# Kernel tuning notes

Hardware: AMD Instinct MI355X
Metric: run time of the kernel (lower is better)

## Reference

```python
import jax, jax.numpy as jnp
import numpy as np

B, S, D, H, DFF = 2, 4096, 768, 12, 3072
DH = D // H
EPS = 1e-6


def layer_norm(x, gamma, beta):
    # torch.std is unbiased (ddof=1); normalizer is (sigma + eps), NOT sqrt(var+eps)
    mu = jnp.mean(x, axis=-1, keepdims=True)
    sigma = jnp.sqrt(jnp.var(x, axis=-1, keepdims=True, ddof=1))
    return gamma * (x - mu) / (sigma + EPS) + beta


def setup_inputs() -> dict:
    key = jax.random.key(0)
    ks = jax.random.split(key, 12)
    sc = 1.0 / np.sqrt(D)
    inp = {
        "x": jax.random.normal(ks[0], (B, S, D), dtype=jnp.float32),
        "mask": jnp.ones((B, S, S), dtype=jnp.float32),  # multiplicative mask
        "wq": jax.random.normal(ks[1], (D, D), dtype=jnp.float32) * sc,
        "bq": jnp.zeros((D,), dtype=jnp.float32),
        "wk": jax.random.normal(ks[2], (D, D), dtype=jnp.float32) * sc,
        "bk": jnp.zeros((D,), dtype=jnp.float32),
        "wv": jax.random.normal(ks[3], (D, D), dtype=jnp.float32) * sc,
        "bv": jnp.zeros((D,), dtype=jnp.float32),
        "wo": jax.random.normal(ks[4], (D, D), dtype=jnp.float32) * sc,
        "bo": jnp.zeros((D,), dtype=jnp.float32),
        "w1": jax.random.normal(ks[5], (D, DFF), dtype=jnp.float32) * sc,
        "b1": jnp.zeros((DFF,), dtype=jnp.float32),
        "w2": jax.random.normal(ks[6], (DFF, D), dtype=jnp.float32) * (1.0 / np.sqrt(DFF)),
        "b2": jnp.zeros((D,), dtype=jnp.float32),
        "gamma1": jnp.ones((D,), dtype=jnp.float32),
        "beta1": jnp.zeros((D,), dtype=jnp.float32),
        "gamma2": jnp.ones((D,), dtype=jnp.float32),
        "beta2": jnp.zeros((D,), dtype=jnp.float32),
    }
    return inp


def reference(x, mask, wq, bq, wk, bk, wv, bv, wo, bo, w1, b1, w2, b2,
              gamma1, beta1, gamma2, beta2):
    # Pre-LN encoder layer (is_pre_layer_norm=True); dropout is identity (eval).
    l1 = layer_norm(x, gamma1, beta1)                      # [B,S,D]

    # --- multi-head self-attention ---
    q = (l1 @ wq + bq).reshape(B, S, H, DH).transpose(0, 2, 1, 3)  # [B,H,S,DH]
    k = (l1 @ wk + bk).reshape(B, S, H, DH).transpose(0, 2, 1, 3)
    v = (l1 @ wv + bv).reshape(B, S, H, DH).transpose(0, 2, 1, 3)
    scores = jnp.einsum("bhqd,bhkd->bhqk", q, k) / jnp.sqrt(jnp.float32(DH))
    scores = scores * mask[:, None, :, :]                  # multiplicative mask, pre-softmax
    attn = jax.nn.softmax(scores, axis=-1)                 # [B,H,S,S]
    ctx = jnp.einsum("bhqk,bhkd->bhqd", attn, v)           # [B,H,S,DH]
    ctx = ctx.transpose(0, 2, 1, 3).reshape(B, S, D)       # [B,S,D]
    a = ctx  # NOTE: original forward never applies out_linear in attention()... it does in forward
    a = ctx
    # MultiHeadAttention.forward returns the merged heads WITHOUT out_linear applied?
    # Re-check: forward() reshapes and returns `output` without out_linear in given code.
    x1 = x + a                                             # residual

    l2 = layer_norm(x1, gamma2, beta2)
    h = jax.nn.relu(l2 @ w1 + b1) @ w2 + b2                # FFN
    return h + x1
```

## Files before the change

kernel.cpp:

```cpp
#include <hip/hip_runtime.h>
#include <cstdint>
#include <cstddef>

#define BB   2
#define SEQ  4096
#define DD   768
#define HH   12
#define DHH  64
#define DFFN 3072
#define NTOK (BB*SEQ)

using bf16x8 = __attribute__((ext_vector_type(8))) __bf16;
using f32x4  = __attribute__((ext_vector_type(4))) float;
typedef unsigned int u32;

#define QK_SCALE 0.18033688011112042f

__device__ __forceinline__ float fast_exp2(float x) {
    return __builtin_amdgcn_exp2f(x);
}

__device__ __forceinline__ unsigned short f2bf(float f) {
    unsigned u = __float_as_uint(f);
    u = u + 0x7FFFu + ((u >> 16) & 1u);
    return (unsigned short)(u >> 16);
}
__device__ __forceinline__ unsigned short f2bf_trunc(float f) {
    return (unsigned short)(__float_as_uint(f) >> 16);
}

__device__ __forceinline__ bf16x8 ld_bf8(const unsigned short* p) {
    return *(const bf16x8*)p;
}

__device__ __forceinline__ void gl_lds16(const unsigned short* g, unsigned short* l) {
    __builtin_amdgcn_global_load_lds(
        (const __attribute__((address_space(1))) u32*)(uintptr_t)(const void*)g,
        (__attribute__((address_space(3))) u32*)(uintptr_t)(void*)l,
        16, 0, 0);
}

template <int N>
__device__ __forceinline__ float dpp_ror(float x) {
    return __int_as_float(__builtin_amdgcn_update_dpp(
        0, __float_as_int(x), 0x120 | N, 0xf, 0xf, false));
}
__device__ __forceinline__ float rowmax16(float x) {
    x = fmaxf(x, dpp_ror<1>(x));
    x = fmaxf(x, dpp_ror<2>(x));
    x = fmaxf(x, dpp_ror<4>(x));
    x = fmaxf(x, dpp_ror<8>(x));
    return x;
}
__device__ __forceinline__ float rowsum16(float x) {
    x += dpp_ror<1>(x);
    x += dpp_ror<2>(x);
    x += dpp_ror<4>(x);
    x += dpp_ror<8>(x);
    return x;
}

__global__ __launch_bounds__(256) void transpose_qkv_to_bf16(
    const float* __restrict__ wq, const float* __restrict__ wk, const float* __restrict__ wv,
    unsigned short* __restrict__ dst)
{
    __shared__ float tile[32][33];
    const int z = blockIdx.z;
    const float* src = (z == 0) ? wq : (z == 1 ? wk : wv);
    const float scale = (z == 0) ? QK_SCALE : 1.0f;
    unsigned short* d = dst + (size_t)z * 768 * 768;
    const int c0 = blockIdx.x * 32, r0 = blockIdx.y * 32;
    const int tx = threadIdx.x, ty = threadIdx.y;
#pragma unroll
    for (int i = 0; i < 32; i += 8)
        tile[ty + i][tx] = src[(size_t)(r0 + ty + i) * 768 + c0 + tx];
    __syncthreads();
#pragma unroll
    for (int i = 0; i < 32; i += 8)
        d[(size_t)(c0 + ty + i) * 768 + r0 + tx] = f2bf(scale * tile[tx][ty + i]);
}

__global__ __launch_bounds__(256) void transpose_f32_to_bf16(
    const float* __restrict__ src, unsigned short* __restrict__ dst, int R, int C, float scale)
{
    __shared__ float tile[32][33];
    const int c0 = blockIdx.x * 32, r0 = blockIdx.y * 32;
    const int tx = threadIdx.x, ty = threadIdx.y;
#pragma unroll
    for (int i = 0; i < 32; i += 8)
        tile[ty + i][tx] = src[(size_t)(r0 + ty + i) * C + c0 + tx];
    __syncthreads();
#pragma unroll
    for (int i = 0; i < 32; i += 8)
        dst[(size_t)(c0 + ty + i) * R + r0 + tx] = f2bf(scale * tile[tx][ty + i]);
}

__global__ void concat_bias(const float* __restrict__ bq, const float* __restrict__ bk,
                            const float* __restrict__ bv, float* __restrict__ bqkv)
{
    int i = blockIdx.x * 256 + threadIdx.x;
    if (i < 3 * DD)
        bqkv[i] = (i < DD) ? bq[i] * QK_SCALE : (i < 2 * DD ? bk[i - DD] : bv[i - 2 * DD]);
}

__global__ __launch_bounds__(256) void mask_check(const float* __restrict__ mask, int* __restrict__ flag)
{
    const size_t n = (size_t)BB * SEQ * SEQ;
    const size_t stride = (size_t)gridDim.x * 1024;
    int bad = 0;
    for (size_t i = ((size_t)blockIdx.x * 256 + threadIdx.x) * 4; i < n; i += stride) {
        float4 v = *(const float4*)&mask[i];
        bad |= (v.x != 1.f) | (v.y != 1.f) | (v.z != 1.f) | (v.w != 1.f);
    }
    if (bad) atomicOr(flag, 1);
}

__global__ __launch_bounds__(256) void ln_fused(
    const float* __restrict__ x, const float* __restrict__ add,
    const float* __restrict__ gamma, const float* __restrict__ beta,
    unsigned short* __restrict__ out_ln, float* __restrict__ x1out)
{
    const int row = blockIdx.x, t = threadIdx.x;
    const size_t base = (size_t)row * DD;
    float v[3], s = 0.f, sq = 0.f;
#pragma unroll
    for (int p = 0; p < 3; ++p) {
        int idx = t + p * 256;
        float val = x[base + idx];
        if (add) val += add[base + idx];
        v[p] = val; s += val; sq += val * val;
    }
#pragma unroll
    for (int off = 1; off < 64; off <<= 1) {
        s  += __shfl_xor(s,  off);
        sq += __shfl_xor(sq, off);
    }
    __shared__ float red[8];
    const int wave = t >> 6;
    if ((t & 63) == 0) { red[wave] = s; red[4 + wave] = sq; }
    __syncthreads();
    s  = red[0] + red[1] + red[2] + red[3];
    sq = red[4] + red[5] + red[6] + red[7];
    const float mu   = s * (1.f / 768.f);
    const float var  = fmaxf((sq - 768.f * mu * mu) * (1.f / 767.f), 0.f);
    const float rstd = 1.f / (sqrtf(var) + 1e-6f);
#pragma unroll
    for (int p = 0; p < 3; ++p) {
        int idx = t + p * 256;
        if (x1out) x1out[base + idx] = v[p];
        out_ln[base + idx] = f2bf(gamma[idx] * (v[p] - mu) * rstd + beta[idx]);
    }
}

__global__ __launch_bounds__(256) void gemm_bf16(
    const unsigned short* __restrict__ A, const unsigned short* __restrict__ Bt,
    const float* __restrict__ bias, const float* __restrict__ resid,
    unsigned short* __restrict__ outB, float* __restrict__ outF,
    int M, int N, int K, int relu)
{
    __shared__ __align__(16) unsigned short As[128][64];
    __shared__ __align__(16) unsigned short Bs[128][64];
    const int tid = threadIdx.x;
    const int lane = tid & 63, wave = tid >> 6;
    const int quad = lane >> 4, l16 = lane & 15;
    const int wm = wave >> 1, wn = wave & 1;

    int wg = blockIdx.y * gridDim.x + blockIdx.x;
    const int nwg = gridDim.x * gridDim.y;
    wg = (wg & 7) * (nwg >> 3) + (wg >> 3);
    const int m0 = (wg / gridDim.x) * 128, n0 = (wg % gridDim.x) * 128;

    const f32x4 fzero = {0.f, 0.f, 0.f, 0.f};
    f32x4 acc[4][4];
#pragma unroll
    for (int i = 0; i < 4; ++i)
#pragma unroll
        for (int j = 0; j < 4; ++j) acc[i][j] = fzero;

    const int r  = tid >> 3;
    const int cg = tid & 7;

    for (int k0 = 0; k0 < K; k0 += 64) {
#pragma unroll
        for (int rr = 0; rr < 4; ++rr) {
            const int row = r + rr * 32;
            const int gc8 = (cg ^ (row & 7)) * 8;
            gl_lds16(&A [(size_t)(m0 + row) * K + k0 + gc8], &As[row][cg * 8]);
            gl_lds16(&Bt[(size_t)(n0 + row) * K + k0 + gc8], &Bs[row][cg * 8]);
        }
        __syncthreads();
#pragma unroll
        for (int ks = 0; ks < 2; ++ks) {
            bf16x8 af[4], bfv[4];
#pragma unroll
            for (int i = 0; i < 4; ++i) {
                const int row = wm * 64 + i * 16 + l16;
                af[i] = ld_bf8(&As[row][((ks * 4 + quad) ^ (row & 7)) * 8]);
            }
#pragma unroll
            for (int j = 0; j < 4; ++j) {
                const int row = wn * 64 + j * 16 + l16;
                bfv[j] = ld_bf8(&Bs[row][((ks * 4 + quad) ^ (row & 7)) * 8]);
            }
#pragma unroll
            for (int i = 0; i < 4; ++i)
#pragma unroll
                for (int j = 0; j < 4; ++j)
                    acc[i][j] = __builtin_amdgcn_mfma_f32_16x16x32_bf16(af[i], bfv[j], acc[i][j], 0, 0, 0);
        }
        __syncthreads();
    }
#pragma unroll
    for (int i = 0; i < 4; ++i)
#pragma unroll
        for (int j = 0; j < 4; ++j)
#pragma unroll
            for (int rr = 0; rr < 4; ++rr) {
                const int gm = m0 + wm * 64 + i * 16 + quad * 4 + rr;
                const int gn = n0 + wn * 64 + j * 16 + l16;
                float v = acc[i][j][rr] + bias[gn];
                if (relu) v = fmaxf(v, 0.f);
                if (resid) v += resid[(size_t)gm * N + gn];
                if (outF) outF[(size_t)gm * N + gn] = v;
                if (outB) outB[(size_t)gm * N + gn] = f2bf(v);
            }
}

__global__ __launch_bounds__(256) void vt_extract(
    const unsigned short* __restrict__ qkv, unsigned short* __restrict__ vtg)
{
    __shared__ unsigned short tile[64][72];
    const int bh = blockIdx.x, b = bh / HH, h = bh % HH;
    const int s0 = blockIdx.y * 64;
    const int tid = threadIdx.x;
#pragma unroll
    for (int p = 0; p < 2; ++p) {
        int idx = tid + p * 256;
        int r = idx >> 3, ch8 = (idx & 7) * 8;
        *(uint4*)&tile[r][ch8] =
            *(const uint4*)&qkv[(size_t)(b * SEQ + s0 + r) * 2304 + 1536 + h * 64 + ch8];
    }
    __syncthreads();
#pragma unroll
    for (int p = 0; p < 2; ++p) {
        int idx = tid + p * 256;
        int d = idx >> 3, sc = (idx & 7) * 8;
        unsigned short tmp[8];
#pragma unroll
        for (int j = 0; j < 8; ++j) tmp[j] = tile[sc + j][d];
        *(uint4*)&vtg[((size_t)bh * 64 + d) * SEQ + s0 + sc] = *(uint4*)tmp;
    }
}

__global__ __launch_bounds__(256, 3) void flash_attn10(
    const unsigned short* __restrict__ qkv, const unsigned short* __restrict__ vtg,
    const float* __restrict__ mask, const int* __restrict__ maskflag,
    float* __restrict__ ctx)
{
    __shared__ __align__(16) unsigned short smem[26112];
    unsigned short (* const Ks)[72]  = (unsigned short (*)[72])smem;
    unsigned short (* const Vt)[136] = (unsigned short (*)[136])(smem + 17408);

    const int tid = threadIdx.x;
    const int lane = tid & 63, wave = tid >> 6;
    const int quad = lane >> 4, l16 = lane & 15;
    unsigned short* const Pw = smem + wave * 4352;

    const int wg  = blockIdx.y * 32 + blockIdx.x;
    const int swz = (wg & 7) * 96 + (wg >> 3);
    const int bh = swz >> 5, b = bh / HH, h = bh % HH;
    const int qbase = (swz & 31) * 128 + wave * 32;
    const int use_mask = *maskflag;

    bf16x8 qf[2][2];
#pragma unroll
    for (int mt = 0; mt < 2; ++mt) {
        const size_t qrow = (size_t)(b * SEQ + qbase + mt * 16 + l16) * 2304 + h * 64;
        qf[mt][0] = ld_bf8(&qkv[qrow + quad * 8]);
        qf[mt][1] = ld_bf8(&qkv[qrow + 32 + quad * 8]);
    }
    const f32x4 fzero = {0.f, 0.f, 0.f, 0.f};
    float l_run[2][4];
    f32x4 o[2][4];
#pragma unroll
    for (int mt = 0; mt < 2; ++mt)
#pragma unroll
        for (int r = 0; r < 4; ++r) { l_run[mt][r] = 0.f; o[mt][r] = fzero; }

    const float* mbase = mask + (size_t)b * SEQ * SEQ;
    const unsigned short* kgbase = qkv + (size_t)b * SEQ * 2304 + 768 + h * 64;
    const unsigned short* vgbase = vtg + (size_t)bh * 64 * SEQ;

    const int sr  = tid >> 3, sc8 = (tid & 7) * 8;
    const int vd  = tid >> 4, vc8 = (tid & 15) * 8;

#define STAGE_NOW(K0_) do {                                                           \
    uint4 kb[4], vb[4];                                                               \
    _Pragma("unroll")                                                                 \
    for (int p = 0; p < 4; ++p)                                                       \
        kb[p] = *(const uint4*)&kgbase[(size_t)((K0_) + sr + p * 32) * 2304 + sc8];   \
    _Pragma("unroll")                                                                 \
    for (int p = 0; p < 4; ++p)                                                       \
        vb[p] = *(const uint4*)&vgbase[(size_t)(vd + p * 16) * SEQ + (K0_) + vc8];    \
    _Pragma("unroll")                                                                 \
    for (int p = 0; p < 4; ++p) *(uint4*)&Ks[sr + p * 32][sc8] = kb[p];               \
    _Pragma("unroll")                                                                 \
    for (int p = 0; p < 4; ++p) *(uint4*)&Vt[vd + p * 16][vc8] = vb[p];               \
} while (0)

    STAGE_NOW(0);
    __syncthreads();

    if (!use_mask) {
        float lsum[2][4];
#pragma unroll
        for (int mt = 0; mt < 2; ++mt)
#pragma unroll
            for (int r = 0; r < 4; ++r) lsum[mt][r] = 0.f;

        for (int t = 0; t < SEQ / 128; ++t) {
            f32x4 st[2][8];
#pragma unroll
            for (int j = 0; j < 8; ++j) {
                bf16x8 kf0 = ld_bf8(&Ks[j * 16 + l16][quad * 8]);
                bf16x8 kf1 = ld_bf8(&Ks[j * 16 + l16][32 + quad * 8]);
                st[0][j] = __builtin_amdgcn_mfma_f32_16x16x32_bf16(qf[0][0], kf0, fzero, 0, 0, 0);
                st[0][j] = __builtin_amdgcn_mfma_f32_16x16x32_bf16(qf[0][1], kf1, st[0][j], 0, 0, 0);
                st[1][j] = __builtin_amdgcn_mfma_f32_16x16x32_bf16(qf[1][0], kf0, fzero, 0, 0, 0);
                st[1][j] = __builtin_amdgcn_mfma_f32_16x16x32_bf16(qf[1][1], kf1, st[1][j], 0, 0, 0);
            }
            __syncthreads();
#pragma unroll
            for (int mt = 0; mt < 2; ++mt) {
#pragma unroll
                for (int r = 0; r < 4; ++r) {
                    float acc = 0.f;
#pragma unroll
                    for (int j = 0; j < 8; ++j) {
                        float p = fast_exp2(st[mt][j][r]);
                        st[mt][j][r] = p;
                        acc += p;
                    }
                    lsum[mt][r] += acc;
                }
#pragma unroll
                for (int j = 0; j < 8; ++j)
#pragma unroll
                    for (int r = 0; r < 4; ++r)
                        Pw[mt * 2176 + (quad * 4 + r) * 136 + j * 16 + l16] =
                            f2bf_trunc(st[mt][j][r]);
            }
#pragma unroll
            for (int kk = 0; kk < 4; ++kk) {
                bf16x8 pf0 = ld_bf8(&Pw[l16 * 136 + kk * 32 + quad * 8]);
                bf16x8 pf1 = ld_bf8(&Pw[2176 + l16 * 136 + kk * 32 + quad * 8]);
#pragma unroll
                for (int v = 0; v < 4; ++v) {
                    bf16x8 vf = ld_bf8(&Vt[v * 16 + l16][kk * 32 + quad * 8]);
                    o[0][v] = __builtin_amdgcn_mfma_f32_16x16x32_bf16(pf0, vf, o[0][v], 0, 0, 0);
                    o[1][v] = __builtin_amdgcn_mfma_f32_16x16x32_bf16(pf1, vf, o[1][v], 0, 0, 0);
                }
            }
            __syncthreads();
            if (t < SEQ / 128 - 1) {
                STAGE_NOW((t + 1) * 128);
                __syncthreads();
            }
        }
#pragma unroll
        for (int mt = 0; mt < 2; ++mt)
#pragma unroll
            for (int r = 0; r < 4; ++r) l_run[mt][r] = rowsum16(lsum[mt][r]);
    } else {
        float m_run[2][4];
#pragma unroll
        for (int mt = 0; mt < 2; ++mt)
#pragma unroll
            for (int r = 0; r < 4; ++r) m_run[mt][r] = -1e30f;

        for (int t = 0; t < SEQ / 128; ++t) {
            const int k0 = t * 128;
            f32x4 st[2][8];
#pragma unroll
            for (int j = 0; j < 8; ++j) {
                bf16x8 kf0 = ld_bf8(&Ks[j * 16 + l16][quad * 8]);
                bf16x8 kf1 = ld_bf8(&Ks[j * 16 + l16][32 + quad * 8]);
                st[0][j] = __builtin_amdgcn_mfma_f32_16x16x32_bf16(qf[0][0], kf0, fzero, 0, 0, 0);
                st[0][j] = __builtin_amdgcn_mfma_f32_16x16x32_bf16(qf[0][1], kf1, st[0][j], 0, 0, 0);
                st[1][j] = __builtin_amdgcn_mfma_f32_16x16x32_bf16(qf[1][0], kf0, fzero, 0, 0, 0);
                st[1][j] = __builtin_amdgcn_mfma_f32_16x16x32_bf16(qf[1][1], kf1, st[1][j], 0, 0, 0);
            }
            __syncthreads();
#pragma unroll
            for (int mt = 0; mt < 2; ++mt) {
                const int qr = qbase + mt * 16 + quad * 4;
#pragma unroll
                for (int r = 0; r < 4; ++r) {
                    const float* mrow = &mbase[(size_t)(qr + r) * SEQ + k0 + l16];
#pragma unroll
                    for (int j = 0; j < 8; ++j)
                        st[mt][j][r] *= mrow[j * 16];
                }
            }
#pragma unroll
            for (int mt = 0; mt < 2; ++mt) {
                float alpha[4];
#pragma unroll
                for (int r = 0; r < 4; ++r) {
                    float mx = st[mt][0][r];
#pragma unroll
                    for (int j = 1; j < 8; ++j) mx = fmaxf(mx, st[mt][j][r]);
                    mx = rowmax16(mx);
                    const float mnew = fmaxf(m_run[mt][r], mx);
                    alpha[r] = fast_exp2(m_run[mt][r] - mnew);
                    float ssum = 0.f;
#pragma unroll
                    for (int j = 0; j < 8; ++j) {
                        st[mt][j][r] = fast_exp2(st[mt][j][r] - mnew);
                        ssum += st[mt][j][r];
                    }
                    ssum = rowsum16(ssum);
                    l_run[mt][r] = l_run[mt][r] * alpha[r] + ssum;
                    m_run[mt][r] = mnew;
                }
#pragma unroll
                for (int v = 0; v < 4; ++v)
#pragma unroll
                    for (int r = 0; r < 4; ++r) o[mt][v][r] *= alpha[r];
#pragma unroll
                for (int j = 0; j < 8; ++j)
#pragma unroll
                    for (int r = 0; r < 4; ++r)
                        Pw[mt * 2176 + (quad * 4 + r) * 136 + j * 16 + l16] =
                            f2bf_trunc(st[mt][j][r]);
            }
#pragma unroll
            for (int kk = 0; kk < 4; ++kk) {
                bf16x8 pf0 = ld_bf8(&Pw[l16 * 136 + kk * 32 + quad * 8]);
                bf16x8 pf1 = ld_bf8(&Pw[2176 + l16 * 136 + kk * 32 + quad * 8]);
#pragma unroll
                for (int v = 0; v < 4; ++v) {
                    bf16x8 vf = ld_bf8(&Vt[v * 16 + l16][kk * 32 + quad * 8]);
                    o[0][v] = __builtin_amdgcn_mfma_f32_16x16x32_bf16(pf0, vf, o[0][v], 0, 0, 0);
                    o[1][v] = __builtin_amdgcn_mfma_f32_16x16x32_bf16(pf1, vf, o[1][v], 0, 0, 0);
                }
            }
            __syncthreads();
            if (t < SEQ / 128 - 1) {
                STAGE_NOW((t + 1) * 128);
                __syncthreads();
            }
        }
    }
#undef STAGE_NOW

#pragma unroll
    for (int mt = 0; mt < 2; ++mt)
#pragma unroll
        for (int v = 0; v < 4; ++v)
#pragma unroll
            for (int r = 0; r < 4; ++r) {
                const int row = qbase + mt * 16 + quad * 4 + r;
                ctx[(size_t)(b * SEQ + row) * DD + h * 64 + v * 16 + l16] =
                    o[mt][v][r] / l_run[mt][r];
            }
}

extern "C" void kernel_launch(void* const* d_in, const int* in_sizes, int n_in,
                              void* d_out, int out_size, void* d_ws, size_t ws_size,
                              hipStream_t stream)
{
    (void)in_sizes; (void)n_in; (void)out_size; (void)ws_size;
    const float* x      = (const float*)d_in[0];
    const float* mask   = (const float*)d_in[1];
    const float* wq     = (const float*)d_in[2];
    const float* bq     = (const float*)d_in[3];
    const float* wk     = (const float*)d_in[4];
    const float* bk     = (const float*)d_in[5];
    const float* wv     = (const float*)d_in[6];
    const float* bv     = (const float*)d_in[7];
    const float* w1     = (const float*)d_in[10];
    const float* b1     = (const float*)d_in[11];
    const float* w2     = (const float*)d_in[12];
    const float* b2     = (const float*)d_in[13];
    const float* gamma1 = (const float*)d_in[14];
    const float* beta1  = (const float*)d_in[15];
    const float* gamma2 = (const float*)d_in[16];
    const float* beta2  = (const float*)d_in[17];
    float* out = (float*)d_out;

    char* ws = (char*)d_ws;
    size_t off = 0;
    auto take = [&](size_t bytes) -> char* {
        char* p = ws + off;
        off = (off + bytes + 255) & ~(size_t)255;
        return p;
    };
    unsigned short* wqkvT = (unsigned short*)take((size_t)2304 * 768 * 2);
    unsigned short* w1T   = (unsigned short*)take((size_t)3072 * 768 * 2);
    unsigned short* w2T   = (unsigned short*)take((size_t)768 * 3072 * 2);
    float*          bqkv  = (float*)take(2304 * 4);
    int*            mflag = (int*)take(256);
    unsigned short* l12   = (unsigned short*)take((size_t)NTOK * DD * 2);
    unsigned short* qkv   = (unsigned short*)take((size_t)NTOK * 2304 * 2);
    float*          x1    = (float*)take((size_t)NTOK * DD * 4);
    char*           big   = take((size_t)NTOK * DFFN * 2);
    float*          ctx   = (float*)big;
    unsigned short* vtg   = (unsigned short*)(big + (size_t)NTOK * DD * 4);
    unsigned short* hb    = (unsigned short*)big;

    (void)hipMemsetAsync(mflag, 0, 4, stream);
    mask_check<<<2048, 256, 0, stream>>>(mask, mflag);

    transpose_qkv_to_bf16<<<dim3(24, 24, 3), dim3(32, 8), 0, stream>>>(wq, wk, wv, wqkvT);
    transpose_f32_to_bf16<<<dim3(96, 24), dim3(32, 8), 0, stream>>>(w1, w1T, 768, 3072, 1.0f);
    transpose_f32_to_bf16<<<dim3(24, 96), dim3(32, 8), 0, stream>>>(w2, w2T, 3072, 768, 1.0f);
    concat_bias<<<9, 256, 0, stream>>>(bq, bk, bv, bqkv);

    ln_fused<<<NTOK, 256, 0, stream>>>(x, nullptr, gamma1, beta1, l12, nullptr);
    gemm_bf16<<<dim3(2304 / 128, NTOK / 128), 256, 0, stream>>>(
        l12, wqkvT, bqkv, nullptr, qkv, nullptr, NTOK, 2304, 768, 0);
    vt_extract<<<dim3(BB * HH, SEQ / 64), 256, 0, stream>>>(qkv, vtg);
    flash_attn10<<<dim3(SEQ / 128, BB * HH), 256, 0, stream>>>(qkv, vtg, mask, mflag, ctx);
    ln_fused<<<NTOK, 256, 0, stream>>>(x, ctx, gamma2, beta2, l12, x1);
    gemm_bf16<<<dim3(3072 / 128, NTOK / 128), 256, 0, stream>>>(
        l12, w1T, b1, nullptr, hb, nullptr, NTOK, 3072, 768, 1);
    gemm_bf16<<<dim3(768 / 128, NTOK / 128), 256, 0, stream>>>(
        hb, w2T, b2, x1, nullptr, out, NTOK, 768, 3072, 0);
}
```

Baseline: 619.0 us.

## Keep attention probabilities in registers via transposed QK^T MFMA layout

Swaps the MFMA operand order for S = K·Q^T so each lane holds score values along the key dimension. That layout lets P be packed directly into bf16 A-operands for the PV MFMA, removing the per-wave LDS round trip for P. V fragments are now gathered with two 8-byte LDS reads to match the new k ordering. Row max and sum reductions use cross-quad shuffles instead of DPP row ops, and one barrier per tile is dropped by moving the sync to the loop top. The trade is strided V loads and extra shuffles for alpha and l, in exchange for less LDS traffic and fewer barriers.

```diff
diff --git a/kernel.cpp b/kernel.cpp
--- a/kernel.cpp
+++ b/kernel.cpp
@@ -33,31 +33,26 @@
     return *(const bf16x8*)p;
 }
 
+__device__ __forceinline__ bf16x8 pack_bf8(f32x4 a, f32x4 b) {
+    union { u32 w[4]; bf16x8 v; } u;
+    u.w[0] = (u32)f2bf_trunc(a[0]) | ((u32)f2bf_trunc(a[1]) << 16);
+    u.w[1] = (u32)f2bf_trunc(a[2]) | ((u32)f2bf_trunc(a[3]) << 16);
+    u.w[2] = (u32)f2bf_trunc(b[0]) | ((u32)f2bf_trunc(b[1]) << 16);
+    u.w[3] = (u32)f2bf_trunc(b[2]) | ((u32)f2bf_trunc(b[3]) << 16);
+    return u.v;
+}
+__device__ __forceinline__ bf16x8 vfrag(const unsigned short* lo, const unsigned short* hi) {
+    union { uint2 d[2]; bf16x8 v; } u;
+    u.d[0] = *(const uint2*)lo;
+    u.d[1] = *(const uint2*)hi;
+    return u.v;
+}
+
 __device__ __forceinline__ void gl_lds16(const unsigned short* g, unsigned short* l) {
     __builtin_amdgcn_global_load_lds(
         (const __attribute__((address_space(1))) u32*)(uintptr_t)(const void*)g,
         (__attribute__((address_space(3))) u32*)(uintptr_t)(void*)l,
         16, 0, 0);
-}
-
-template <int N>
-__device__ __forceinline__ float dpp_ror(float x) {
-    return __int_as_float(__builtin_amdgcn_update_dpp(
-        0, __float_as_int(x), 0x120 | N, 0xf, 0xf, false));
-}
-__device__ __forceinline__ float rowmax16(float x) {
-    x = fmaxf(x, dpp_ror<1>(x));
-    x = fmaxf(x, dpp_ror<2>(x));
-    x = fmaxf(x, dpp_ror<4>(x));
-    x = fmaxf(x, dpp_ror<8>(x));
-    return x;
-}
-__device__ __forceinline__ float rowsum16(float x) {
-    x += dpp_ror<1>(x);
-    x += dpp_ror<2>(x);
-    x += dpp_ror<4>(x);
-    x += dpp_ror<8>(x);
-    return x;
 }
 
 __global__ __launch_bounds__(256) void transpose_qkv_to_bf16(
@@ -252,19 +247,17 @@
     }
 }
 
-__global__ __launch_bounds__(256, 3) void flash_attn10(
+__global__ __launch_bounds__(256, 3) void flash_attn11(
     const unsigned short* __restrict__ qkv, const unsigned short* __restrict__ vtg,
     const float* __restrict__ mask, const int* __restrict__ maskflag,
     float* __restrict__ ctx)
 {
-    __shared__ __align__(16) unsigned short smem[26112];
-    unsigned short (* const Ks)[72]  = (unsigned short (*)[72])smem;
-    unsigned short (* const Vt)[136] = (unsigned short (*)[136])(smem + 17408);
+    __shared__ __align__(16) unsigned short Ks[128][72];
+    __shared__ __align__(16) unsigned short Vt[64][136];
 
     const int tid = threadIdx.x;
     const int lane = tid & 63, wave = tid >> 6;
     const int quad = lane >> 4, l16 = lane & 15;
-    unsigned short* const Pw = smem + wave * 4352;
 
     const int wg  = blockIdx.y * 32 + blockIdx.x;
     const int swz = (wg & 7) * 96 + (wg >> 3);
@@ -280,12 +273,12 @@
         qf[mt][1] = ld_bf8(&qkv[qrow + 32 + quad * 8]);
     }
     const f32x4 fzero = {0.f, 0.f, 0.f, 0.f};
-    float l_run[2][4];
+    float l_run[2] = {0.f, 0.f};
     f32x4 o[2][4];
 #pragma unroll
     for (int mt = 0; mt < 2; ++mt)
 #pragma unroll
-        for (int r = 0; r < 4; ++r) { l_run[mt][r] = 0.f; o[mt][r] = fzero; }
+        for (int r = 0; r < 4; ++r) o[mt][r] = fzero;
 
     const float* mbase = mask + (size_t)b * SEQ * SEQ;
     const unsigned short* kgbase = qkv + (size_t)b * SEQ * 2304 + 768 + h * 64;
@@ -308,162 +301,133 @@
     for (int p = 0; p < 4; ++p) *(uint4*)&Vt[vd + p * 16][vc8] = vb[p];               \
 } while (0)
 
+#define QKT_TILE() do {                                                               \
+    _Pragma("unroll")                                                                 \
+    for (int j = 0; j < 8; ++j) {                                                     \
+        bf16x8 kf0 = ld_bf8(&Ks[j * 16 + l16][quad * 8]);                             \
+        bf16x8 kf1 = ld_bf8(&Ks[j * 16 + l16][32 + quad * 8]);                        \
+        st[0][j] = __builtin_amdgcn_mfma_f32_16x16x32_bf16(kf0, qf[0][0], fzero, 0, 0, 0); \
+        st[0][j] = __builtin_amdgcn_mfma_f32_16x16x32_bf16(kf1, qf[0][1], st[0][j], 0, 0, 0); \
+        st[1][j] = __builtin_amdgcn_mfma_f32_16x16x32_bf16(kf0, qf[1][0], fzero, 0, 0, 0); \
+        st[1][j] = __builtin_amdgcn_mfma_f32_16x16x32_bf16(kf1, qf[1][1], st[1][j], 0, 0, 0); \
+    }                                                                                 \
+} while (0)
+
+#define PV_TILE() do {                                                                \
+    _Pragma("unroll")                                                                 \
+    for (int kk = 0; kk < 4; ++kk) {                                                  \
+        bf16x8 pa0 = pack_bf8(st[0][2 * kk], st[0][2 * kk + 1]);                      \
+        bf16x8 pa1 = pack_bf8(st[1][2 * kk], st[1][2 * kk + 1]);                      \
+        _Pragma("unroll")                                                             \
+        for (int v = 0; v < 4; ++v) {                                                 \
+            const unsigned short* vrow = &Vt[v * 16 + l16][kk * 32 + quad * 4];       \
+            bf16x8 vf = vfrag(vrow, vrow + 16);                                       \
+            o[0][v] = __builtin_amdgcn_mfma_f32_16x16x32_bf16(pa0, vf, o[0][v], 0, 0, 0); \
+            o[1][v] = __builtin_amdgcn_mfma_f32_16x16x32_bf16(pa1, vf, o[1][v], 0, 0, 0); \
+        }                                                                             \
+    }                                                                                 \
+} while (0)
+
     STAGE_NOW(0);
-    __syncthreads();
 
     if (!use_mask) {
-        float lsum[2][4];
-#pragma unroll
-        for (int mt = 0; mt < 2; ++mt)
-#pragma unroll
-            for (int r = 0; r < 4; ++r) lsum[mt][r] = 0.f;
-
         for (int t = 0; t < SEQ / 128; ++t) {
+            __syncthreads();
             f32x4 st[2][8];
-#pragma unroll
-            for (int j = 0; j < 8; ++j) {
-                bf16x8 kf0 = ld_bf8(&Ks[j * 16 + l16][quad * 8]);
-                bf16x8 kf1 = ld_bf8(&Ks[j * 16 + l16][32 + quad * 8]);
-                st[0][j] = __builtin_amdgcn_mfma_f32_16x16x32_bf16(qf[0][0], kf0, fzero, 0, 0, 0);
-                st[0][j] = __builtin_amdgcn_mfma_f32_16x16x32_bf16(qf[0][1], kf1, st[0][j], 0, 0, 0);
-                st[1][j] = __builtin_amdgcn_mfma_f32_16x16x32_bf16(qf[1][0], kf0, fzero, 0, 0, 0);
-                st[1][j] = __builtin_amdgcn_mfma_f32_16x16x32_bf16(qf[1][1], kf1, st[1][j], 0, 0, 0);
-            }
-            __syncthreads();
+            QKT_TILE();
 #pragma unroll
             for (int mt = 0; mt < 2; ++mt) {
-#pragma unroll
-                for (int r = 0; r < 4; ++r) {
-                    float acc = 0.f;
-#pragma unroll
-                    for (int j = 0; j < 8; ++j) {
+                float acc = 0.f;
+#pragma unroll
+                for (int j = 0; j < 8; ++j)
+#pragma unroll
+                    for (int r = 0; r < 4; ++r) {
                         float p = fast_exp2(st[mt][j][r]);
                         st[mt][j][r] = p;
                         acc += p;
                     }
-                    lsum[mt][r] += acc;
-                }
-#pragma unroll
-                for (int j = 0; j < 8; ++j)
-#pragma unroll
-                    for (int r = 0; r < 4; ++r)
-                        Pw[mt * 2176 + (quad * 4 + r) * 136 + j * 16 + l16] =
-                            f2bf_trunc(st[mt][j][r]);
-            }
-#pragma unroll
-            for (int kk = 0; kk < 4; ++kk) {
-                bf16x8 pf0 = ld_bf8(&Pw[l16 * 136 + kk * 32 + quad * 8]);
-                bf16x8 pf1 = ld_bf8(&Pw[2176 + l16 * 136 + kk * 32 + quad * 8]);
-#pragma unroll
-                for (int v = 0; v < 4; ++v) {
-                    bf16x8 vf = ld_bf8(&Vt[v * 16 + l16][kk * 32 + quad * 8]);
-                    o[0][v] = __builtin_amdgcn_mfma_f32_16x16x32_bf16(pf0, vf, o[0][v], 0, 0, 0);
-                    o[1][v] = __builtin_amdgcn_mfma_f32_16x16x32_bf16(pf1, vf, o[1][v], 0, 0, 0);
-                }
-            }
+                l_run[mt] += acc;
+            }
+            PV_TILE();
             __syncthreads();
-            if (t < SEQ / 128 - 1) {
-                STAGE_NOW((t + 1) * 128);
-                __syncthreads();
-            }
+            if (t < SEQ / 128 - 1) STAGE_NOW((t + 1) * 128);
         }
 #pragma unroll
-        for (int mt = 0; mt < 2; ++mt)
-#pragma unroll
-            for (int r = 0; r < 4; ++r) l_run[mt][r] = rowsum16(lsum[mt][r]);
+        for (int mt = 0; mt < 2; ++mt) {
+            l_run[mt] += __shfl_xor(l_run[mt], 16);
+            l_run[mt] += __shfl_xor(l_run[mt], 32);
+        }
     } else {
-        float m_run[2][4];
-#pragma unroll
-        for (int mt = 0; mt < 2; ++mt)
-#pragma unroll
-            for (int r = 0; r < 4; ++r) m_run[mt][r] = -1e30f;
-
+        float m_run[2] = {-1e30f, -1e30f};
         for (int t = 0; t < SEQ / 128; ++t) {
             const int k0 = t * 128;
+            __syncthreads();
             f32x4 st[2][8];
-#pragma unroll
-            for (int j = 0; j < 8; ++j) {
-                bf16x8 kf0 = ld_bf8(&Ks[j * 16 + l16][quad * 8]);
-                bf16x8 kf1 = ld_bf8(&Ks[j * 16 + l16][32 + quad * 8]);
-                st[0][j] = __builtin_amdgcn_mfma_f32_16x16x32_bf16(qf[0][0], kf0, fzero, 0, 0, 0);
-                st[0][j] = __builtin_amdgcn_mfma_f32_16x16x32_bf16(qf[0][1], kf1, st[0][j], 0, 0, 0);
-                st[1][j] = __builtin_amdgcn_mfma_f32_16x16x32_bf16(qf[1][0], kf0, fzero, 0, 0, 0);
-                st[1][j] = __builtin_amdgcn_mfma_f32_16x16x32_bf16(qf[1][1], kf1, st[1][j], 0, 0, 0);
-            }
-            __syncthreads();
+            QKT_TILE();
 #pragma unroll
             for (int mt = 0; mt < 2; ++mt) {
-                const int qr = qbase + mt * 16 + quad * 4;
-#pragma unroll
-                for (int r = 0; r < 4; ++r) {
-                    const float* mrow = &mbase[(size_t)(qr + r) * SEQ + k0 + l16];
-#pragma unroll
-                    for (int j = 0; j < 8; ++j)
-                        st[mt][j][r] *= mrow[j * 16];
-                }
+                const float* mrow =
+                    &mbase[(size_t)(qbase + mt * 16 + l16) * SEQ + k0 + quad * 4];
+#pragma unroll
+                for (int j = 0; j < 8; ++j)
+#pragma unroll
+                    for (int r = 0; r < 4; ++r)
+                        st[mt][j][r] *= mrow[j * 16 + r];
             }
 #pragma unroll
             for (int mt = 0; mt < 2; ++mt) {
-                float alpha[4];
-#pragma unroll
-                for (int r = 0; r < 4; ++r) {
-                    float mx = st[mt][0][r];
-#pragma unroll
-                    for (int j = 1; j < 8; ++j) mx = fmaxf(mx, st[mt][j][r]);
-                    mx = rowmax16(mx);
-                    const float mnew = fmaxf(m_run[mt][r], mx);
-                    alpha[r] = fast_exp2(m_run[mt][r] - mnew);
-                    float ssum = 0.f;
-#pragma unroll
-                    for (int j = 0; j < 8; ++j) {
+                float mx = st[mt][0][0];
+#pragma unroll
+                for (int j = 0; j < 8; ++j)
+#pragma unroll
+                    for (int r = 0; r < 4; ++r) mx = fmaxf(mx, st[mt][j][r]);
+                mx = fmaxf(mx, __shfl_xor(mx, 16));
+                mx = fmaxf(mx, __shfl_xor(mx, 32));
+                const float mnew = fmaxf(m_run[mt], mx);
+                const float alpha = fast_exp2(m_run[mt] - mnew);
+                float ssum = 0.f;
+#pragma unroll
+                for (int j = 0; j < 8; ++j)
+#pragma unroll
+                    for (int r = 0; r < 4; ++r) {
                         st[mt][j][r] = fast_exp2(st[mt][j][r] - mnew);
                         ssum += st[mt][j][r];
                     }
-                    ssum = rowsum16(ssum);
-                    l_run[mt][r] = l_run[mt][r] * alpha[r] + ssum;
-                    m_run[mt][r] = mnew;
-                }
+                ssum += __shfl_xor(ssum, 16);
+                ssum += __shfl_xor(ssum, 32);
+                l_run[mt] = l_run[mt] * alpha + ssum;
+                m_run[mt] = mnew;
+                float aq[4];
+#pragma unroll
+                for (int r = 0; r < 4; ++r) aq[r] = __shfl(alpha, quad * 4 + r);
 #pragma unroll
                 for (int v = 0; v < 4; ++v)
 #pragma unroll
-                    for (int r = 0; r < 4; ++r) o[mt][v][r] *= alpha[r];
-#pragma unroll
-                for (int j = 0; j < 8; ++j)
-#pragma unroll
-                    for (int r = 0; r < 4; ++r)
-                        Pw[mt * 2176 + (quad * 4 + r) * 136 + j * 16 + l16] =
-                            f2bf_trunc(st[mt][j][r]);
-            }
-#pragma unroll
-            for (int kk = 0; kk < 4; ++kk) {
-                bf16x8 pf0 = ld_bf8(&Pw[l16 * 136 + kk * 32 + quad * 8]);
-                bf16x8 pf1 = ld_bf8(&Pw[2176 + l16 * 136 + kk * 32 + quad * 8]);
-#pragma unroll
-                for (int v = 0; v < 4; ++v) {
-                    bf16x8 vf = ld_bf8(&Vt[v * 16 + l16][kk * 32 + quad * 8]);
-                    o[0][v] = __builtin_amdgcn_mfma_f32_16x16x32_bf16(pf0, vf, o[0][v], 0, 0, 0);
-                    o[1][v] = __builtin_amdgcn_mfma_f32_16x16x32_bf16(pf1, vf, o[1][v], 0, 0, 0);
-                }
-            }
+                    for (int r = 0; r < 4; ++r) o[mt][v][r] *= aq[r];
+            }
+            PV_TILE();
             __syncthreads();
-            if (t < SEQ / 128 - 1) {
-                STAGE_NOW((t + 1) * 128);
-                __syncthreads();
-            }
+            if (t < SEQ / 128 - 1) STAGE_NOW((t + 1) * 128);
         }
     }
 #undef STAGE_NOW
-
-#pragma unroll
-    for (int mt = 0; mt < 2; ++mt)
+#undef QKT_TILE
+#undef PV_TILE
+
+#pragma unroll
+    for (int mt = 0; mt < 2; ++mt) {
+        float lq[4];
+#pragma unroll
+        for (int r = 0; r < 4; ++r) lq[r] = __shfl(l_run[mt], quad * 4 + r);
 #pragma unroll
         for (int v = 0; v < 4; ++v)
 #pragma unroll
             for (int r = 0; r < 4; ++r) {
                 const int row = qbase + mt * 16 + quad * 4 + r;
                 ctx[(size_t)(b * SEQ + row) * DD + h * 64 + v * 16 + l16] =
-                    o[mt][v][r] / l_run[mt][r];
-            }
+                    o[mt][v][r] / lq[r];
+            }
+    }
 }
 
 extern "C" void kernel_launch(void* const* d_in, const int* in_sizes, int n_in,
@@ -521,7 +485,7 @@
     gemm_bf16<<<dim3(2304 / 128, NTOK / 128), 256, 0, stream>>>(
         l12, wqkvT, bqkv, nullptr, qkv, nullptr, NTOK, 2304, 768, 0);
     vt_extract<<<dim3(BB * HH, SEQ / 64), 256, 0, stream>>>(qkv, vtg);
-    flash_attn10<<<dim3(SEQ / 128, BB * HH), 256, 0, stream>>>(qkv, vtg, mask, mflag, ctx);
+    flash_attn11<<<dim3(SEQ / 128, BB * HH), 256, 0, stream>>>(qkv, vtg, mask, mflag, ctx);
     ln_fused<<<NTOK, 256, 0, stream>>>(x, ctx, gamma2, beta2, l12, x1);
     gemm_bf16<<<dim3(3072 / 128, NTOK / 128), 256, 0, stream>>>(
         l12, w1T, b1, nullptr, hb, nullptr, NTOK, 3072, 768, 1);
```

Result: faster. 588.7 us (-4.9%).
